# Performance work log

Hardware: AMD Instinct MI355X
Metric: run time of the kernel (lower is better)

## Reference

```python
import jax, jax.numpy as jnp
import numpy as np
from jax import lax

NEG_INF = -10000.0  # matches the torch code's fill value


def setup_inputs() -> dict:
    key = jax.random.key(0)
    k1, k2, k3 = jax.random.split(key, 3)
    B, T, L = 512, 512, 102  # n_labels = vocab_size(100) + 2
    logits = jax.random.normal(k1, (B, T, L), dtype=jnp.float32)
    transitions = jax.random.normal(k2, (L, L), dtype=jnp.float32)
    lens = jax.random.randint(k3, (B,), 0, 512, dtype=jnp.int32)
    return {"logits": logits, "transitions": transitions, "lens": lens}


def reference(logits, transitions, lens):
    """Linear-chain CRF partition function (forward algorithm).

    logits: [B, T, L] emission scores (L = n_labels incl. start/stop)
    transitions: [L, L], transitions[j, k] = score of k -> j
    lens: [B] int sequence lengths
    returns: [B] log partition function
    """
    B, T, L = logits.shape
    start_idx, stop_idx = L - 2, L - 1

    alpha0 = jnp.full((B, L), NEG_INF, dtype=logits.dtype).at[:, start_idx].set(0.0)

    def step(carry, logit_t):
        alpha, c_lens = carry  # alpha: [B, L], logit_t: [B, L]
        # mat[b, j, k] = transitions[j, k] + alpha[b, k]
        mat = transitions[None, :, :] + alpha[:, None, :]
        alpha_nxt = logit_t + jax.scipy.special.logsumexp(mat, axis=2)  # [B, L]
        alive = (c_lens > 0)[:, None]
        alpha = jnp.where(alive, alpha_nxt, alpha)
        return (alpha, c_lens - 1), None

    (alpha, _), _ = lax.scan(step, (alpha0, lens), jnp.swapaxes(logits, 0, 1))

    alpha = alpha + transitions[stop_idx][None, :]
    norm = jax.scipy.special.logsumexp(alpha, axis=1)  # [B]
    return norm
```

## Files before the change

### kernel.cpp

```cpp
#include <hip/hip_runtime.h>


typedef _Float16 half2_t __attribute__((ext_vector_type(2)));

#define CRF_L 102
#define CRF_RP 104
#define CRF_START 100
#define CRF_STOP 101
#define NEG_BIG (-1.0e30f)
#define LN2F 0.6931471805599453f

#define REP13(X) X(0) X(1) X(2) X(3) X(4) X(5) X(6) X(7) X(8) X(9) X(10) X(11) X(12)

#define FDOT2(a, b, c) __builtin_amdgcn_fdot2((a), (b), (c), false)

template <int CTRL>
__device__ __forceinline__ float dpp_add_step(float x) {
    int xi = __builtin_bit_cast(int, x);
    int yi = __builtin_amdgcn_update_dpp(0, xi, CTRL, 0xf, 0xf, true);
    return x + __builtin_bit_cast(float, yi);
}
__device__ __forceinline__ float wave_sum64(float v) {
    v = dpp_add_step<0x111>(v);
    v = dpp_add_step<0x112>(v);
    v = dpp_add_step<0x114>(v);
    v = dpp_add_step<0x118>(v);
    v = dpp_add_step<0x142>(v);
    v = dpp_add_step<0x143>(v);
    return __builtin_bit_cast(float,
        __builtin_amdgcn_readlane(__builtin_bit_cast(int, v), 63));
}

__device__ __forceinline__ half2_t mk2(const float* rowp, int k, float rmx) {
    float e0 = (k + 0 < CRF_L) ? __expf(rowp[k + 0] - rmx) : 0.f;
    float e1 = (k + 1 < CRF_L) ? __expf(rowp[k + 1] - rmx) : 0.f;
    return (half2_t){(_Float16)e0, (_Float16)e1};
}

__attribute__((amdgpu_waves_per_eu(1, 1)))
__launch_bounds__(64)
__global__ void crf_forward_kernel(const float* __restrict__ logits,
                                   const float* __restrict__ trans,
                                   const int* __restrict__ lens,
                                   float* __restrict__ out,
                                   int B, int T) {
    const int b    = blockIdx.x;
    const int lane = threadIdx.x;
    const int r0   = 2 * lane;
    const int r1   = 2 * lane + 1;
    const bool valid = (lane < 51);

    __shared__ __align__(16) float TS[CRF_L * CRF_RP];
    __shared__ __align__(16) _Float16 Q[112];

    #pragma unroll 4
    for (int r = 0; r < CRF_L; ++r)
        for (int c = lane; c < CRF_L; c += 64)
            TS[CRF_RP * r + c] = trans[CRF_L * r + c];

    if (lane < 56) {
        int i0 = 2 * lane;
        Q[i0]     = (_Float16)((i0 == CRF_START) ? 1.f : 0.f);
        Q[i0 + 1] = (_Float16)0.f;
    }
    __builtin_amdgcn_wave_barrier();

    const float* rowA = &TS[CRF_RP * (valid ? r0 : 0)];
    const float* rowB = &TS[CRF_RP * (valid ? r1 : 0)];
    float rmax0 = NEG_BIG, rmax1 = NEG_BIG;
    #pragma unroll
    for (int k = 0; k < CRF_L; ++k) {
        rmax0 = fmaxf(rmax0, rowA[k]);
        rmax1 = fmaxf(rmax1, rowB[k]);
    }

#define DECLM(j) half2_t ma##j##_0, ma##j##_1, ma##j##_2, ma##j##_3, \
                         mb##j##_0, mb##j##_1, mb##j##_2, mb##j##_3;
    REP13(DECLM)
#undef DECLM
#define PACKJ(j) \
    ma##j##_0 = mk2(rowA, 8*(j)+0, rmax0); ma##j##_1 = mk2(rowA, 8*(j)+2, rmax0); \
    ma##j##_2 = mk2(rowA, 8*(j)+4, rmax0); ma##j##_3 = mk2(rowA, 8*(j)+6, rmax0); \
    mb##j##_0 = mk2(rowB, 8*(j)+0, rmax1); mb##j##_1 = mk2(rowB, 8*(j)+2, rmax1); \
    mb##j##_2 = mk2(rowB, 8*(j)+4, rmax1); mb##j##_3 = mk2(rowB, 8*(j)+6, rmax1);
    REP13(PACKJ)
#undef PACKJ

    const float erm0 = (valid)              ? rmax0 : NEG_BIG;
    const float erm1 = (valid && r1 < CRF_L) ? rmax1 : NEG_BIG;

    const int len = min(lens[b], T);
    const float* lg = logits + (size_t)b * (size_t)T * (size_t)CRF_L;
    const int loff = valid ? r0 : 0;

    float2 l0 = *reinterpret_cast<const float2*>(lg + loff);
    float2 lgB = *reinterpret_cast<const float2*>(lg + (size_t)min(1, T - 1) * CRF_L + loff);
    float2 lgC = *reinterpret_cast<const float2*>(lg + (size_t)min(2, T - 1) * CRF_L + loff);
    float2 Ec = make_float2(__expf(l0.x + erm0), __expf(l0.y + erm1));

    float invRs = 0.00390625f;
    float log2Rs = 0.f;
    float Lacc = 0.f;
    float q0 = 0.f, q1 = 0.f;
    const int sidx = min(r0, 102);

    for (int t = 0; t < len; ++t) {
        const float4* P4 = reinterpret_cast<const float4*>(&Q[0]);
        float c0 = 0.f, c1 = 0.f, c2 = 0.f, c3 = 0.f;
        float d0 = 0.f, d1 = 0.f, d2 = 0.f, d3 = 0.f;
#define DOT(j) { float4 q = P4[j]; \
        half2_t q0h = __builtin_bit_cast(half2_t, q.x); \
        half2_t q1h = __builtin_bit_cast(half2_t, q.y); \
        half2_t q2h = __builtin_bit_cast(half2_t, q.z); \
        half2_t q3h = __builtin_bit_cast(half2_t, q.w); \
        c0 = FDOT2(ma##j##_0, q0h, c0); c1 = FDOT2(ma##j##_1, q1h, c1); \
        c2 = FDOT2(ma##j##_2, q2h, c2); c3 = FDOT2(ma##j##_3, q3h, c3); \
        d0 = FDOT2(mb##j##_0, q0h, d0); d1 = FDOT2(mb##j##_1, q1h, d1); \
        d2 = FDOT2(mb##j##_2, q2h, d2); d3 = FDOT2(mb##j##_3, q3h, d3); }
        REP13(DOT)
#undef DOT
        float dot0 = (c0 + c1) + (c2 + c3);
        float dot1 = (d0 + d1) + (d2 + d3);

        Lacc += log2Rs + 8.0f;
        q0 = (dot0 * Ec.x) * invRs;
        q1 = (dot1 * Ec.y) * invRs;

        __builtin_amdgcn_wave_barrier();
        *reinterpret_cast<half2_t*>(&Q[sidx]) =
            (half2_t){(_Float16)q0, (_Float16)q1};
        __builtin_amdgcn_wave_barrier();

        float R = wave_sum64(q0 + q1);
        R = fmaxf(R, 1e-30f);
        invRs = __builtin_amdgcn_rcpf(R) * 0.00390625f;
        log2Rs = __log2f(R);

        Ec.x = __expf(lgB.x + erm0);
        Ec.y = __expf(lgB.y + erm1);
        lgB = lgC;
        lgC = *reinterpret_cast<const float2*>(lg + (size_t)min(t + 3, T - 1) * CRF_L + loff);
    }

    float ts0 = TS[CRF_RP * CRF_STOP + (valid ? r0 : 0)];
    float ts1 = TS[CRF_RP * CRF_STOP + (valid ? r1 : 0)];
    float e;
    if (len == 0) {
        e = ((r0 == CRF_START) ? __expf(ts0) : 0.f);
    } else {
        e = q0 * __expf(ts0) + q1 * __expf(ts1);
    }
    float se = wave_sum64(e);

    if (lane == 0) out[b] = LN2F * Lacc + __logf(se);
}

extern "C" void kernel_launch(void* const* d_in, const int* in_sizes, int n_in,
                              void* d_out, int out_size, void* d_ws, size_t ws_size,
                              hipStream_t stream) {
    const float* logits = (const float*)d_in[0];
    const float* trans  = (const float*)d_in[1];
    const int*   lens   = (const int*)d_in[2];
    float* out = (float*)d_out;

    const int B = 512;
    const int T = 512;

    crf_forward_kernel<<<dim3(B), dim3(64), 0, stream>>>(
        logits, trans, lens, out, B, T);
}
```

Before: 408.3 us.

## Interleave wave reduction and exp work with dot-product chain in CRF recurrence

Moves the per-step DPP wave sum of the previous alpha, the reciprocal/log2, and the emission exp computations into the loop body. They are interleaved between the 13 unrolled fdot2 groups, so their latency hides behind the independent dot-product work instead of sitting serially after the LDS store. Initial state handling is restructured so the normalisation of step t-1 is computed at the start of step t. The constant per-step log offset is hoisted out of the loop and applied once at the end. The risk is that the compiler reorders the interleaving anyway, or that register pressure increases.

```diff
diff --git a/kernel.cpp b/kernel.cpp
--- a/kernel.cpp
+++ b/kernel.cpp
@@ -93,15 +93,13 @@
     const float* lg = logits + (size_t)b * (size_t)T * (size_t)CRF_L;
     const int loff = valid ? r0 : 0;
 
-    float2 l0 = *reinterpret_cast<const float2*>(lg + loff);
+    float2 lgA = *reinterpret_cast<const float2*>(lg + loff);
     float2 lgB = *reinterpret_cast<const float2*>(lg + (size_t)min(1, T - 1) * CRF_L + loff);
     float2 lgC = *reinterpret_cast<const float2*>(lg + (size_t)min(2, T - 1) * CRF_L + loff);
-    float2 Ec = make_float2(__expf(l0.x + erm0), __expf(l0.y + erm1));
 
-    float invRs = 0.00390625f;
-    float log2Rs = 0.f;
+    float q0 = (r0 == CRF_START) ? 1.f : 0.f;
+    float q1 = 0.f;
     float Lacc = 0.f;
-    float q0 = 0.f, q1 = 0.f;
     const int sidx = min(r0, 102);
 
     for (int t = 0; t < len; ++t) {
@@ -117,29 +115,49 @@
         c2 = FDOT2(ma##j##_2, q2h, c2); c3 = FDOT2(ma##j##_3, q3h, c3); \
         d0 = FDOT2(mb##j##_0, q0h, d0); d1 = FDOT2(mb##j##_1, q1h, d1); \
         d2 = FDOT2(mb##j##_2, q2h, d2); d3 = FDOT2(mb##j##_3, q3h, d3); }
-        REP13(DOT)
+        DOT(0)
+        DOT(1)
+        float s = q0 + q1;
+        DOT(2)
+        s = dpp_add_step<0x111>(s);
+        DOT(3)
+        s = dpp_add_step<0x112>(s);
+        DOT(4)
+        s = dpp_add_step<0x114>(s);
+        DOT(5)
+        s = dpp_add_step<0x118>(s);
+        DOT(6)
+        s = dpp_add_step<0x142>(s);
+        DOT(7)
+        s = dpp_add_step<0x143>(s);
+        DOT(8)
+        float R = __builtin_bit_cast(float,
+            __builtin_amdgcn_readlane(__builtin_bit_cast(int, s), 63));
+        DOT(9)
+        R = fmaxf(R, 1e-30f);
+        float invRs = __builtin_amdgcn_rcpf(R) * 0.00390625f;
+        DOT(10)
+        float l2R = __log2f(R);
+        DOT(11)
+        float ecx = __expf(lgA.x + erm0);
+        float ecy = __expf(lgA.y + erm1);
+        DOT(12)
 #undef DOT
+        lgA = lgB; lgB = lgC;
+        lgC = *reinterpret_cast<const float2*>(
+            lg + (size_t)min(t + 3, T - 1) * CRF_L + loff);
+
         float dot0 = (c0 + c1) + (c2 + c3);
         float dot1 = (d0 + d1) + (d2 + d3);
 
-        Lacc += log2Rs + 8.0f;
-        q0 = (dot0 * Ec.x) * invRs;
-        q1 = (dot1 * Ec.y) * invRs;
+        Lacc += l2R;
+        q0 = (dot0 * ecx) * invRs;
+        q1 = (dot1 * ecy) * invRs;
 
         __builtin_amdgcn_wave_barrier();
         *reinterpret_cast<half2_t*>(&Q[sidx]) =
             (half2_t){(_Float16)q0, (_Float16)q1};
         __builtin_amdgcn_wave_barrier();
-
-        float R = wave_sum64(q0 + q1);
-        R = fmaxf(R, 1e-30f);
-        invRs = __builtin_amdgcn_rcpf(R) * 0.00390625f;
-        log2Rs = __log2f(R);
-
-        Ec.x = __expf(lgB.x + erm0);
-        Ec.y = __expf(lgB.y + erm1);
-        lgB = lgC;
-        lgC = *reinterpret_cast<const float2*>(lg + (size_t)min(t + 3, T - 1) * CRF_L + loff);
     }
 
     float ts0 = TS[CRF_RP * CRF_STOP + (valid ? r0 : 0)];
@@ -152,7 +170,8 @@
     }
     float se = wave_sum64(e);
 
-    if (lane == 0) out[b] = LN2F * Lacc + __logf(se);
+    if (lane == 0)
+        out[b] = LN2F * (Lacc + 8.0f * (float)len) + __logf(se);
 }
 
 extern "C" void kernel_launch(void* const* d_in, const int* in_sizes, int n_in,
```

Result: slower. 441.1 us (+8.0%).
